# Optimization experiments

Measured on AMD Instinct MI355X. Metric: run time of the kernel, lower is better.

Reference implementation:

```python
import jax, jax.numpy as jnp
import numpy as np

IN_F = 4096
OUT_F = 4096
BATCH = 1024

def setup_inputs() -> dict:
    key = jax.random.key(0)
    k = jax.random.split(key, 7)
    x = jax.random.normal(k[0], (BATCH, IN_F), dtype=jnp.float32)
    weight_mu = jax.random.normal(k[1], (OUT_F, IN_F), dtype=jnp.float32) * (1.0 / np.sqrt(IN_F))
    # torch init: uniform(-5,-3) for sigma params (raw values, used directly as std)
    weight_sigma = jax.random.uniform(k[2], (OUT_F, IN_F), dtype=jnp.float32, minval=-5.0, maxval=-3.0)
    bias_mu = jnp.zeros((OUT_F,), dtype=jnp.float32)
    bias_sigma = jax.random.uniform(k[3], (OUT_F,), dtype=jnp.float32, minval=-5.0, maxval=-3.0)
    eps_w = jax.random.normal(k[4], (OUT_F, IN_F), dtype=jnp.float32)
    eps_b = jax.random.normal(k[5], (OUT_F,), dtype=jnp.float32)
    return {"x": x, "weight_mu": weight_mu, "weight_sigma": weight_sigma,
            "bias_mu": bias_mu, "bias_sigma": bias_sigma,
            "eps_w": eps_w, "eps_b": eps_b}

def reference(x, weight_mu, weight_sigma, bias_mu, bias_sigma, eps_w, eps_b):
    # training-mode forward: reparameterized weight sample then dense matmul
    weight = weight_mu + eps_w * weight_sigma        # [out, in]
    bias = bias_mu + eps_b * bias_sigma              # [out]
    # F.linear(x, W, b) = x @ W.T + b
    return jnp.einsum('bi,oi->bo', x, weight) + bias
```

## Files before the change

### kernel.cpp

```cpp
#include <hip/hip_runtime.h>
#include <hip/hip_bf16.h>
#include <hip/hip_cooperative_groups.h>
#include <stdint.h>

namespace cg = cooperative_groups;

#define M_BATCH 1024
#define N_OUT   4096
#define K_IN    4096

#define BM 128
#define BN 128
#define BK 64
#define KPER  (K_IN / 2)
#define KITER (KPER / BK)

typedef __attribute__((ext_vector_type(8))) __bf16 bf16x8_t;
typedef __attribute__((ext_vector_type(4))) float f32x4_t;
typedef __attribute__((ext_vector_type(4))) float fvec4;

__device__ __forceinline__ unsigned short f2bf_bits(float f) {
    union { __hip_bfloat16 h; unsigned short u; } cvt;
    cvt.h = __float2bfloat16(f);
    return cvt.u;
}

struct __align__(16) US8 { unsigned short s[8]; };

__global__ __launch_bounds__(512, 2) void fused_kernel(
    const float* __restrict__ x,
    const float* __restrict__ wmu,
    const float* __restrict__ wsig,
    const float* __restrict__ bmu,
    const float* __restrict__ bsig,
    const float* __restrict__ epsw,
    const float* __restrict__ epsb,
    unsigned short* __restrict__ wb,
    unsigned short* __restrict__ xb,
    float* __restrict__ C)
{
    __shared__ unsigned short lds[2 * 32768];

    const int t  = threadIdx.x;
    const int bx = blockIdx.x;
    const int bn = bx & 31;
    const int bm = bx >> 5;

    {
        const size_t base4 = (size_t)bn * 131072 + (size_t)bm * 16384;
        const size_t base8 = (size_t)bn * 65536  + (size_t)bm * 8192;
        const fvec4* mu4 = (const fvec4*)wmu;
        const fvec4* sg4 = (const fvec4*)wsig;
        const fvec4* ep4 = (const fvec4*)epsw;
        US8* wb8 = (US8*)wb;
        #pragma unroll
        for (int c = 0; c < 16; ++c) {
            const int u = c * 512 + t;
            const size_t i4 = base4 + (size_t)u * 2;
            fvec4 m0 = __builtin_nontemporal_load(mu4 + i4);
            fvec4 m1 = __builtin_nontemporal_load(mu4 + i4 + 1);
            fvec4 s0 = __builtin_nontemporal_load(sg4 + i4);
            fvec4 s1 = __builtin_nontemporal_load(sg4 + i4 + 1);
            fvec4 e0 = __builtin_nontemporal_load(ep4 + i4);
            fvec4 e1 = __builtin_nontemporal_load(ep4 + i4 + 1);
            US8 o;
            o.s[0] = f2bf_bits(fmaf(e0.x, s0.x, m0.x));
            o.s[1] = f2bf_bits(fmaf(e0.y, s0.y, m0.y));
            o.s[2] = f2bf_bits(fmaf(e0.z, s0.z, m0.z));
            o.s[3] = f2bf_bits(fmaf(e0.w, s0.w, m0.w));
            o.s[4] = f2bf_bits(fmaf(e1.x, s1.x, m1.x));
            o.s[5] = f2bf_bits(fmaf(e1.y, s1.y, m1.y));
            o.s[6] = f2bf_bits(fmaf(e1.z, s1.z, m1.z));
            o.s[7] = f2bf_bits(fmaf(e1.w, s1.w, m1.w));
            wb8[base8 + u] = o;
        }

        const size_t xbase8 = (size_t)bm * 65536 + (size_t)bn * 2048;
        const fvec4* x4 = (const fvec4*)x;
        US8* xb8 = (US8*)xb;
        #pragma unroll
        for (int c = 0; c < 4; ++c) {
            const int u = c * 512 + t;
            const size_t i4 = (xbase8 + u) * 2;
            fvec4 v0 = __builtin_nontemporal_load(x4 + i4);
            fvec4 v1 = __builtin_nontemporal_load(x4 + i4 + 1);
            US8 o;
            o.s[0] = f2bf_bits(v0.x);
            o.s[1] = f2bf_bits(v0.y);
            o.s[2] = f2bf_bits(v0.z);
            o.s[3] = f2bf_bits(v0.w);
            o.s[4] = f2bf_bits(v1.x);
            o.s[5] = f2bf_bits(v1.y);
            o.s[6] = f2bf_bits(v1.z);
            o.s[7] = f2bf_bits(v1.w);
            xb8[xbase8 + u] = o;
        }
    }

    cg::this_grid().sync();

    const unsigned short* A = xb;
    const unsigned short* B = wb;
    const int bm0   = bm * BM;
    const int bn0   = bn * BN;
    const int lane  = t & 63;
    const int wave  = t >> 6;
    const int khalf = wave >> 2;
    const int quadw = wave & 3;
    const int wrow  = (quadw >> 1) * 64;
    const int wcol  = (quadw & 1) * 64;
    const int lm    = lane & 15;
    const int quad  = lane >> 4;

    f32x4_t acc[4][4] = {};

    const unsigned short* srcs[8];
    const int rlow = t >> 3;
    const int jsw  = ((t & 7) ^ (rlow & 7)) * 8;
    #pragma unroll
    for (int s = 0; s < 8; ++s) {
        const int row  = rlow + (s & 1) * 64;
        const int half = (s >> 1) & 1;
        const unsigned short* base = (s < 4)
            ? (A + (size_t)(bm0 + row) * K_IN)
            : (B + (size_t)(bn0 + row) * K_IN);
        srcs[s] = base + half * KPER + jsw;
    }
    char* dst0 = (char*)lds + t * 16;

    #pragma unroll
    for (int s = 0; s < 8; ++s)
        __builtin_amdgcn_global_load_lds(
            (const __attribute__((address_space(1))) void*)(srcs[s]),
            (__attribute__((address_space(3))) void*)(dst0 + s * 8192), 16, 0, 0);

    for (int it = 0; it < KITER; ++it) {
        __syncthreads();

        if (it + 1 < KITER) {
            const int koff = (it + 1) * BK;
            const int nb   = ((it + 1) & 1) * 65536;
            #pragma unroll
            for (int s = 0; s < 8; ++s)
                __builtin_amdgcn_global_load_lds(
                    (const __attribute__((address_space(1))) void*)(srcs[s] + koff),
                    (__attribute__((address_space(3))) void*)(dst0 + nb + s * 8192), 16, 0, 0);
        }

        const unsigned short* Lb = lds + (it & 1) * 32768;
        const unsigned short* Ah = Lb + khalf * 8192;
        const unsigned short* Bh = Lb + 16384 + khalf * 8192;

        #pragma unroll
        for (int kk = 0; kk < 2; ++kk) {
            const int p = ((kk * 4) + quad) ^ (lm & 7);
            bf16x8_t a_frag[4], b_frag[4];
            #pragma unroll
            for (int im = 0; im < 4; im++)
                a_frag[im] = *(const bf16x8_t*)(Ah + ((wrow + im * 16 + lm) * 8 + p) * 8);
            #pragma unroll
            for (int jn = 0; jn < 4; jn++)
                b_frag[jn] = *(const bf16x8_t*)(Bh + ((wcol + jn * 16 + lm) * 8 + p) * 8);
            #pragma unroll
            for (int im = 0; im < 4; im++)
                #pragma unroll
                for (int jn = 0; jn < 4; jn++)
                    acc[im][jn] = __builtin_amdgcn_mfma_f32_16x16x32_bf16(
                        a_frag[im], b_frag[jn], acc[im][jn], 0, 0, 0);
        }
    }

    f32x4_t* red = (f32x4_t*)lds;
    if (wave >= 4) {
        #pragma unroll
        for (int im = 0; im < 4; im++)
            #pragma unroll
            for (int jn = 0; jn < 4; jn++)
                red[quadw * 1024 + (im * 4 + jn) * 64 + lane] = acc[im][jn];
    }
    __syncthreads();
    if (wave < 4) {
        #pragma unroll
        for (int jn = 0; jn < 4; jn++) {
            const int gn = bn0 + wcol + jn * 16 + lm;
            const float bias = bmu[gn] + epsb[gn] * bsig[gn];
            #pragma unroll
            for (int im = 0; im < 4; im++) {
                const f32x4_t part = red[quadw * 1024 + (im * 4 + jn) * 64 + lane];
                const int gm0 = bm0 + wrow + im * 16 + quad * 4;
                #pragma unroll
                for (int r = 0; r < 4; r++)
                    C[(size_t)(gm0 + r) * N_OUT + gn] = acc[im][jn][r] + part[r] + bias;
            }
        }
    }
}

__global__ __launch_bounds__(256) void naive_kernel(
    const float* __restrict__ x, const float* __restrict__ wmu,
    const float* __restrict__ wsig, const float* __restrict__ bmu,
    const float* __restrict__ bsig, const float* __restrict__ epsw,
    const float* __restrict__ epsb, float* __restrict__ out)
{
    const int o = blockIdx.x * blockDim.x + threadIdx.x;
    const int b = blockIdx.y;
    const float4* xr = (const float4*)(x + (size_t)b * K_IN);
    const float4* mr = (const float4*)(wmu + (size_t)o * K_IN);
    const float4* sr = (const float4*)(wsig + (size_t)o * K_IN);
    const float4* er = (const float4*)(epsw + (size_t)o * K_IN);
    float s = 0.f;
    for (int k = 0; k < K_IN / 4; k++) {
        float4 xv = xr[k], m = mr[k], sg = sr[k], e = er[k];
        s += xv.x * fmaf(e.x, sg.x, m.x);
        s += xv.y * fmaf(e.y, sg.y, m.y);
        s += xv.z * fmaf(e.z, sg.z, m.z);
        s += xv.w * fmaf(e.w, sg.w, m.w);
    }
    out[(size_t)b * N_OUT + o] = s + bmu[o] + epsb[o] * bsig[o];
}

extern "C" void kernel_launch(void* const* d_in, const int* in_sizes, int n_in,
                              void* d_out, int out_size, void* d_ws, size_t ws_size,
                              hipStream_t stream)
{
    const float* x    = (const float*)d_in[0];
    const float* wmu  = (const float*)d_in[1];
    const float* wsig = (const float*)d_in[2];
    const float* bmu  = (const float*)d_in[3];
    const float* bsig = (const float*)d_in[4];
    const float* epsw = (const float*)d_in[5];
    const float* epsb = (const float*)d_in[6];
    float* out = (float*)d_out;

    const size_t need = ((size_t)N_OUT * K_IN + (size_t)M_BATCH * K_IN) * sizeof(unsigned short);
    if (ws_size >= need) {
        unsigned short* wb = (unsigned short*)d_ws;
        unsigned short* xb = wb + (size_t)N_OUT * K_IN;
        void* args[] = { (void*)&x, (void*)&wmu, (void*)&wsig, (void*)&bmu,
                         (void*)&bsig, (void*)&epsw, (void*)&epsb,
                         (void*)&wb, (void*)&xb, (void*)&out };
        hipLaunchCooperativeKernel((const void*)fused_kernel,
                                   dim3(256), dim3(512), args, 0, stream);
    } else {
        dim3 grid(N_OUT / 256, M_BATCH);
        naive_kernel<<<grid, 256, 0, stream>>>(x, wmu, wsig, bmu, bsig, epsw, epsb, out);
    }
}
```

Before: 301.4 us.

## Split cooperative fused kernel into separate prep and GEMM launches

Replaces the cooperative-launch kernel, which converted weights and inputs to bf16 and then used a grid-wide sync before the GEMM, with two ordinary launches: a flat elementwise prep kernel over 10240 blocks and a separate GEMM kernel. This drops the grid barrier and the cooperative-launch overhead and lets the prep phase use many more blocks than the 256 resident ones. It also remaps the block index to output tiles in the GEMM. The cost is an extra kernel launch and the loss of any overlap or cache locality between conversion and GEMM.

```diff
diff --git a/kernel.cpp b/kernel.cpp
--- a/kernel.cpp
+++ b/kernel.cpp
@@ -1,9 +1,6 @@
 #include <hip/hip_runtime.h>
 #include <hip/hip_bf16.h>
-#include <hip/hip_cooperative_groups.h>
 #include <stdint.h>
-
-namespace cg = cooperative_groups;
 
 #define M_BATCH 1024
 #define N_OUT   4096
@@ -27,82 +24,72 @@
 
 struct __align__(16) US8 { unsigned short s[8]; };
 
-__global__ __launch_bounds__(512, 2) void fused_kernel(
+__global__ __launch_bounds__(256) void prep_kernel(
     const float* __restrict__ x,
     const float* __restrict__ wmu,
     const float* __restrict__ wsig,
-    const float* __restrict__ bmu,
-    const float* __restrict__ bsig,
     const float* __restrict__ epsw,
-    const float* __restrict__ epsb,
     unsigned short* __restrict__ wb,
-    unsigned short* __restrict__ xb,
-    float* __restrict__ C)
-{
-    __shared__ unsigned short lds[2 * 32768];
-
-    const int t  = threadIdx.x;
-    const int bx = blockIdx.x;
-    const int bn = bx & 31;
-    const int bm = bx >> 5;
-
-    {
-        const size_t base4 = (size_t)bn * 131072 + (size_t)bm * 16384;
-        const size_t base8 = (size_t)bn * 65536  + (size_t)bm * 8192;
+    unsigned short* __restrict__ xb)
+{
+    const size_t u = (size_t)blockIdx.x * blockDim.x + threadIdx.x;
+    const size_t WU = (size_t)2097152;
+
+    if (u < WU) {
         const fvec4* mu4 = (const fvec4*)wmu;
         const fvec4* sg4 = (const fvec4*)wsig;
         const fvec4* ep4 = (const fvec4*)epsw;
-        US8* wb8 = (US8*)wb;
-        #pragma unroll
-        for (int c = 0; c < 16; ++c) {
-            const int u = c * 512 + t;
-            const size_t i4 = base4 + (size_t)u * 2;
-            fvec4 m0 = __builtin_nontemporal_load(mu4 + i4);
-            fvec4 m1 = __builtin_nontemporal_load(mu4 + i4 + 1);
-            fvec4 s0 = __builtin_nontemporal_load(sg4 + i4);
-            fvec4 s1 = __builtin_nontemporal_load(sg4 + i4 + 1);
-            fvec4 e0 = __builtin_nontemporal_load(ep4 + i4);
-            fvec4 e1 = __builtin_nontemporal_load(ep4 + i4 + 1);
-            US8 o;
-            o.s[0] = f2bf_bits(fmaf(e0.x, s0.x, m0.x));
-            o.s[1] = f2bf_bits(fmaf(e0.y, s0.y, m0.y));
-            o.s[2] = f2bf_bits(fmaf(e0.z, s0.z, m0.z));
-            o.s[3] = f2bf_bits(fmaf(e0.w, s0.w, m0.w));
-            o.s[4] = f2bf_bits(fmaf(e1.x, s1.x, m1.x));
-            o.s[5] = f2bf_bits(fmaf(e1.y, s1.y, m1.y));
-            o.s[6] = f2bf_bits(fmaf(e1.z, s1.z, m1.z));
-            o.s[7] = f2bf_bits(fmaf(e1.w, s1.w, m1.w));
-            wb8[base8 + u] = o;
-        }
-
-        const size_t xbase8 = (size_t)bm * 65536 + (size_t)bn * 2048;
+        const size_t i4 = u * 2;
+        fvec4 m0 = __builtin_nontemporal_load(mu4 + i4);
+        fvec4 m1 = __builtin_nontemporal_load(mu4 + i4 + 1);
+        fvec4 s0 = __builtin_nontemporal_load(sg4 + i4);
+        fvec4 s1 = __builtin_nontemporal_load(sg4 + i4 + 1);
+        fvec4 e0 = __builtin_nontemporal_load(ep4 + i4);
+        fvec4 e1 = __builtin_nontemporal_load(ep4 + i4 + 1);
+        US8 o;
+        o.s[0] = f2bf_bits(fmaf(e0.x, s0.x, m0.x));
+        o.s[1] = f2bf_bits(fmaf(e0.y, s0.y, m0.y));
+        o.s[2] = f2bf_bits(fmaf(e0.z, s0.z, m0.z));
+        o.s[3] = f2bf_bits(fmaf(e0.w, s0.w, m0.w));
+        o.s[4] = f2bf_bits(fmaf(e1.x, s1.x, m1.x));
+        o.s[5] = f2bf_bits(fmaf(e1.y, s1.y, m1.y));
+        o.s[6] = f2bf_bits(fmaf(e1.z, s1.z, m1.z));
+        o.s[7] = f2bf_bits(fmaf(e1.w, s1.w, m1.w));
+        ((US8*)wb)[u] = o;
+    } else {
+        const size_t v = u - WU;
         const fvec4* x4 = (const fvec4*)x;
-        US8* xb8 = (US8*)xb;
-        #pragma unroll
-        for (int c = 0; c < 4; ++c) {
-            const int u = c * 512 + t;
-            const size_t i4 = (xbase8 + u) * 2;
-            fvec4 v0 = __builtin_nontemporal_load(x4 + i4);
-            fvec4 v1 = __builtin_nontemporal_load(x4 + i4 + 1);
-            US8 o;
-            o.s[0] = f2bf_bits(v0.x);
-            o.s[1] = f2bf_bits(v0.y);
-            o.s[2] = f2bf_bits(v0.z);
-            o.s[3] = f2bf_bits(v0.w);
-            o.s[4] = f2bf_bits(v1.x);
-            o.s[5] = f2bf_bits(v1.y);
-            o.s[6] = f2bf_bits(v1.z);
-            o.s[7] = f2bf_bits(v1.w);
-            xb8[xbase8 + u] = o;
-        }
-    }
-
-    cg::this_grid().sync();
-
-    const unsigned short* A = xb;
-    const unsigned short* B = wb;
-    const int bm0   = bm * BM;
-    const int bn0   = bn * BN;
+        fvec4 v0 = __builtin_nontemporal_load(x4 + v * 2);
+        fvec4 v1 = __builtin_nontemporal_load(x4 + v * 2 + 1);
+        US8 o;
+        o.s[0] = f2bf_bits(v0.x);
+        o.s[1] = f2bf_bits(v0.y);
+        o.s[2] = f2bf_bits(v0.z);
+        o.s[3] = f2bf_bits(v0.w);
+        o.s[4] = f2bf_bits(v1.x);
+        o.s[5] = f2bf_bits(v1.y);
+        o.s[6] = f2bf_bits(v1.z);
+        o.s[7] = f2bf_bits(v1.w);
+        ((US8*)xb)[v] = o;
+    }
+}
+
+__global__ __launch_bounds__(512, 2) void gemm_bt_kernel(
+    const unsigned short* __restrict__ A,
+    const unsigned short* __restrict__ B,
+    const float* __restrict__ bmu,
+    const float* __restrict__ bsig,
+    const float* __restrict__ ebias,
+    float* __restrict__ C)
+{
+    __shared__ unsigned short lds[2 * 32768];
+
+    const int t   = threadIdx.x;
+    const int b   = blockIdx.x;
+    const int bn  = (b & 7) | (((b >> 3) & 3) << 3);
+    const int bm  = b >> 5;
+    const int bm0 = bm * BM;
+    const int bn0 = bn * BN;
     const int lane  = t & 63;
     const int wave  = t >> 6;
     const int khalf = wave >> 2;
@@ -183,7 +170,7 @@
         #pragma unroll
         for (int jn = 0; jn < 4; jn++) {
             const int gn = bn0 + wcol + jn * 16 + lm;
-            const float bias = bmu[gn] + epsb[gn] * bsig[gn];
+            const float bias = bmu[gn] + ebias[gn] * bsig[gn];
             #pragma unroll
             for (int im = 0; im < 4; im++) {
                 const f32x4_t part = red[quadw * 1024 + (im * 4 + jn) * 64 + lane];
@@ -236,11 +223,8 @@
     if (ws_size >= need) {
         unsigned short* wb = (unsigned short*)d_ws;
         unsigned short* xb = wb + (size_t)N_OUT * K_IN;
-        void* args[] = { (void*)&x, (void*)&wmu, (void*)&wsig, (void*)&bmu,
-                         (void*)&bsig, (void*)&epsw, (void*)&epsb,
-                         (void*)&wb, (void*)&xb, (void*)&out };
-        hipLaunchCooperativeKernel((const void*)fused_kernel,
-                                   dim3(256), dim3(512), args, 0, stream);
+        prep_kernel<<<10240, 256, 0, stream>>>(x, wmu, wsig, epsw, wb, xb);
+        gemm_bt_kernel<<<256, 512, 0, stream>>>(xb, wb, bmu, bsig, epsb, out);
     } else {
         dim3 grid(N_OUT / 256, M_BATCH);
         naive_kernel<<<grid, 256, 0, stream>>>(x, wmu, wsig, bmu, bsig, epsw, epsb, out);
```

Measured after the change: 250.7 us. -16.8%, faster.
